# Performance work log

Measured on AMD Instinct MI355X. Metric: run time of the kernel, lower is better.

## Reference

```python
import jax, jax.numpy as jnp
import numpy as np

B, S, D, H = 4, 2048, 1024, 16
HD = D // H

def setup_inputs() -> dict:
    key = jax.random.key(0)
    ks = jax.random.split(key, 5)
    x = jax.random.normal(ks[0], (B, S, D), dtype=jnp.float32)
    # learned params (torch Linear: y = x @ W.T + b)
    s1 = 1.0 / np.sqrt(D)
    Wqkv = jax.random.uniform(ks[1], (3 * D, D), jnp.float32, -s1, s1)
    bqkv = jax.random.uniform(ks[2], (3 * D,), jnp.float32, -s1, s1)
    Wproj = jax.random.uniform(ks[3], (D, D), jnp.float32, -s1, s1)
    bproj = jax.random.uniform(ks[4], (D,), jnp.float32, -s1, s1)
    # causal mask, broadcast over batch and heads; 0 -> masked
    mask = jnp.tril(jnp.ones((S, S), jnp.int32))[None, None]
    return {"x": x, "Wqkv": Wqkv, "bqkv": bqkv, "Wproj": Wproj, "bproj": bproj, "mask": mask}

def reference(x, Wqkv, bqkv, Wproj, bproj, mask):
    b, s, d = x.shape
    qkv = x @ Wqkv.T + bqkv                      # [B,S,3D]
    qkv = qkv.reshape(b, s, 3, H, HD).transpose(2, 0, 3, 1, 4)  # [3,B,H,S,HD]
    q, k, v = qkv[0], qkv[1], qkv[2]
    scores = jnp.einsum('bhqd,bhkd->bhqk', q, k) / np.sqrt(HD).astype(np.float32)
    scores = jnp.where(mask == 0, -jnp.inf, scores)
    attn = jax.nn.softmax(scores, axis=-1)
    ctx = jnp.einsum('bhqk,bhkd->bhqd', attn, v)  # [B,H,S,HD]
    ctx = ctx.transpose(0, 2, 1, 3).reshape(b, s, d)
    return ctx @ Wproj.T + bproj
```

## Files before the change

kernel.cpp:

```cpp
#include <hip/hip_runtime.h>
#include <stdint.h>

typedef __bf16 bf16;
typedef __bf16 bf16x4 __attribute__((ext_vector_type(4)));
typedef __bf16 bf16x8 __attribute__((ext_vector_type(8)));
typedef float f32x4 __attribute__((ext_vector_type(4)));
typedef short short4v __attribute__((ext_vector_type(4)));

#define NB 4
#define NS 2048
#define ND 1024
#define NH 16
#define NHD 64
#define QSCALE 0.1803368801111204f
#define FMAX   8.0f

typedef const __attribute__((address_space(1))) unsigned GU;
typedef __attribute__((address_space(3))) unsigned LU;

#define WAIT_VM(n) asm volatile("s_waitcnt vmcnt(" #n ")" ::: "memory")
#define BAR() do { asm volatile("" ::: "memory"); __builtin_amdgcn_s_barrier(); \
                   asm volatile("" ::: "memory"); } while (0)

__device__ __forceinline__ bf16x8 load8f(const float* p) {
    float4 a = *(const float4*)p;
    float4 b = *(const float4*)(p + 4);
    bf16x8 r;
    r[0] = (bf16)a.x; r[1] = (bf16)a.y; r[2] = (bf16)a.z; r[3] = (bf16)a.w;
    r[4] = (bf16)b.x; r[5] = (bf16)b.y; r[6] = (bf16)b.z; r[7] = (bf16)b.w;
    return r;
}
__device__ __forceinline__ void store8(bf16* p, bf16x8 v) { *(bf16x8*)p = v; }
__device__ __forceinline__ void store8(float* p, bf16x8 v) {
    float4 a; a.x = (float)v[0]; a.y = (float)v[1]; a.z = (float)v[2]; a.w = (float)v[3];
    float4 b; b.x = (float)v[4]; b.y = (float)v[5]; b.z = (float)v[6]; b.w = (float)v[7];
    *(float4*)p = a; *(float4*)(p + 4) = b;
}

__device__ __forceinline__ f32x4 mfma16(bf16x4 a, bf16x4 b, f32x4 c) {
#ifdef __HIP_DEVICE_COMPILE__
#if __has_builtin(__builtin_amdgcn_mfma_f32_16x16x16bf16_1k)
    return __builtin_amdgcn_mfma_f32_16x16x16bf16_1k(
        __builtin_bit_cast(short4v, a), __builtin_bit_cast(short4v, b), c, 0, 0, 0);
#else
    f32x4 d;
    asm("v_mfma_f32_16x16x16_bf16 %0, %1, %2, %3"
        : "=v"(d) : "v"(a), "v"(b), "v"(c));
    return d;
#endif
#else
    return c;
#endif
}

__device__ __forceinline__ int sw(int row, int col) {
    return row * 72 + (col ^ (((row >> 2) & 3) * 16));
}

__global__ __launch_bounds__(256)
void convert_kernel(const float* __restrict__ s0, bf16* __restrict__ d0, int n0,
                    const float* __restrict__ s1, bf16* __restrict__ d1, int n1,
                    const float* __restrict__ s2, bf16* __restrict__ d2, int n2)
{
    int idx = (blockIdx.x * 256 + threadIdx.x) * 8;
    const float* s; bf16* d;
    if (idx < n0)              { s = s0 + idx;  d = d0 + idx; }
    else if ((idx -= n0) < n1) { s = s1 + idx;  d = d1 + idx; }
    else if ((idx -= n1) < n2) { s = s2 + idx;  d = d2 + idx; }
    else return;
    *(bf16x8*)d = load8f(s);
}

template<typename TO, int MODE>
__device__ __forceinline__ void epi256(
    f32x4 (&acc)[4][4], bf16* Ls, const float* __restrict__ bias,
    TO* __restrict__ O0, bf16* __restrict__ O1, bf16* __restrict__ O2,
    int N, int m0, int n0, int tid)
{
    const int lane = tid & 63;
    const int w = tid >> 6, wm = w >> 2, wn = w & 3;
    const int lr = lane & 15, quad = lane >> 4;
    const int cls = (MODE == 0) ? (n0 >> 10) : 1;

    if (MODE == 0 && cls == 2) {
#pragma unroll
        for (int im = 0; im < 4; ++im) {
            int rowb = wm * 64 + im * 16 + quad * 4;
#pragma unroll
            for (int in = 0; in < 4; ++in) {
                int col = wn * 64 + in * 16 + lr;
                float bv = bias[n0 + col];
                bf16x4 pv;
#pragma unroll
                for (int r = 0; r < 4; ++r) pv[r] = (bf16)(acc[im][in][r] + bv);
                *(bf16x4*)&Ls[col * 136 + rowb] = pv;
            }
        }
        __syncthreads();
        const int b = m0 >> 11, s0 = m0 & 2047;
#pragma unroll
        for (int p = 0; p < 8; ++p) {
            int idx = tid + 512 * p;
            int col = idx >> 4, mg = idx & 15;
            bf16x8 v8 = *(const bf16x8*)&Ls[col * 136 + mg * 8];
            int ncol = n0 + col;
            int h = (ncol >> 6) & 15, hd = ncol & 63;
            *(bf16x8*)&((bf16*)O0)[((size_t)(b * NH + h) * NHD + hd) * NS + s0 + mg * 8] = v8;
        }
    } else {
#pragma unroll
        for (int im = 0; im < 4; ++im) {
            int rowb = wm * 64 + im * 16 + quad * 4;
#pragma unroll
            for (int in = 0; in < 4; ++in) {
                int col = wn * 64 + in * 16 + lr;
                float bv = bias[n0 + col];
#pragma unroll
                for (int r = 0; r < 4; ++r) {
                    float v = acc[im][in][r] + bv;
                    if (MODE == 0 && cls == 0) v *= QSCALE;
                    Ls[(rowb + r) * 264 + col] = (bf16)v;
                }
            }
        }
        __syncthreads();
#pragma unroll
        for (int p = 0; p < 8; ++p) {
            int idx = tid + 512 * p;
            int row = idx >> 5, colg = (idx & 31) * 8;
            bf16x8 v8 = *(const bf16x8*)&Ls[row * 264 + colg];
            if (MODE == 0) {
                int ncol = n0 + colg;
                int h = (ncol >> 6) & 15, hd = ncol & 63;
                int m = m0 + row, b = m >> 11, s = m & 2047;
                bf16* dst = (cls == 0) ? O1 : O2;
                *(bf16x8*)&dst[((size_t)(b * NH + h) * NS + s) * NHD + hd] = v8;
            } else {
                store8(&O0[(size_t)(m0 + row) * N + n0 + colg], v8);
            }
        }
    }
}

template<typename TO, int MODE>
__global__ __launch_bounds__(512, 2)
void gemm256(const bf16* __restrict__ Xp, const bf16* __restrict__ Wp,
             const float* __restrict__ bias, TO* __restrict__ O0,
             bf16* __restrict__ O1, bf16* __restrict__ O2, int N, int K)
{
    __shared__ __align__(16) bf16 L[49152];
    const int tid  = threadIdx.x;
    const int lane = tid & 63;
    const int w    = tid >> 6;
    const int lr   = lane & 15, quad = lane >> 4;
    const int wm   = w >> 2, wn = w & 3;
    const int m0   = blockIdx.y * 128;
    const int n0   = blockIdx.x * 256;

    const int lanep = lane ^ ((lane >> 3) & 7);
    const bf16* gsrc[6]; int ldst[6];
#pragma unroll
    for (int j = 0; j < 6; ++j) {
        int g = w * 6 + j;
        int isA = g < 16;
        int gb = isA ? g : g - 16;
        int c = gb * 64 + lanep;
        int grow = c >> 3, gcol = (c & 7) * 8;
        gsrc[j] = (isA ? Xp + (size_t)(m0 + grow) * K
                       : Wp + (size_t)(n0 + grow) * K) + gcol;
        ldst[j] = (isA ? 0 : 8192) + gb * 512;
    }

#define STAGE256(t) do { const int kofs_ = (t) * 64;                           \
    bf16* Lb_ = &L[((t) & 1) * 24576];                                         \
    _Pragma("unroll")                                                          \
    for (int j = 0; j < 6; ++j)                                                \
        __builtin_amdgcn_global_load_lds((GU*)(gsrc[j] + kofs_),               \
                                         (LU*)&Lb_[ldst[j]], 16, 0, 0); } while (0)

    const int cxor = (lr & 7) * 8;
    const int col0 = (0 * 32 + quad * 8) ^ cxor;
    const int col1 = (1 * 32 + quad * 8) ^ cxor;
    const int arow0 = (wm * 64 + lr) * 64;
    const int brow0 = 8192 + (wn * 64 + lr) * 64;

    f32x4 acc[4][4] = {};
    const int NT = K >> 6;

    STAGE256(0);
    STAGE256(1);
    WAIT_VM(6);
    BAR();

    for (int t = 0; t < NT; ++t) {
        const int db = (t & 1) * 24576;
        bf16x8 afr[2][4], bfr[2][4];
#pragma unroll
        for (int i = 0; i < 4; ++i) {
            afr[0][i] = *(const bf16x8*)&L[db + arow0 + i * 1024 + col0];
            afr[1][i] = *(const bf16x8*)&L[db + arow0 + i * 1024 + col1];
            bfr[0][i] = *(const bf16x8*)&L[db + brow0 + i * 1024 + col0];
            bfr[1][i] = *(const bf16x8*)&L[db + brow0 + i * 1024 + col1];
        }
        __builtin_amdgcn_s_setprio(1);
#pragma unroll
        for (int ks = 0; ks < 2; ++ks)
#pragma unroll
            for (int im = 0; im < 4; ++im)
#pragma unroll
                for (int in = 0; in < 4; ++in)
                    acc[im][in] = __builtin_amdgcn_mfma_f32_16x16x32_bf16(
                        afr[ks][im], bfr[ks][in], acc[im][in], 0, 0, 0);
        __builtin_amdgcn_s_setprio(0);
        BAR();
        if (t + 2 < NT) { STAGE256(t + 2); WAIT_VM(6); }
        else WAIT_VM(0);
        BAR();
    }

    epi256<TO, MODE>(acc, L, bias, O0, O1, O2, N, m0, n0, tid);
}
#undef STAGE256

__global__ __launch_bounds__(256, 3)
void attn_kernel(const bf16* __restrict__ Q, const bf16* __restrict__ K,
                 const bf16* __restrict__ Vt_g, bf16* __restrict__ ctx)
{
    const int jt = 15 - (blockIdx.x >> 6);
    const int bh = blockIdx.x & 63;
    const int b  = bh >> 4, h = bh & 15;
    const int q0 = jt * 128;
    const bf16* Qp = Q + (size_t)bh * NS * NHD;
    const bf16* Kp = K + (size_t)bh * NS * NHD;
    const bf16* Vp = Vt_g + (size_t)bh * NHD * NS;

    __shared__ union {
        struct { bf16 Kh[64 * 72]; bf16 Vh[64 * 72]; } s;
        bf16 QO[128 * 72];
    } u;

    const int tid  = threadIdx.x;
    const int lane = tid & 63;
    const int w    = tid >> 6;
    const int lr   = lane & 15, quad = lane >> 4;

    const int srow = tid >> 3;
    const int sch  = (tid & 7) * 8;

    bf16x8 kreg[2], vreg[2];
#pragma unroll
    for (int i = 0; i < 2; ++i) {
        kreg[i] = *(const bf16x8*)(Kp + (size_t)(srow + 32 * i) * NHD + sch);
        vreg[i] = *(const bf16x8*)(Vp + (size_t)(srow + 32 * i) * NS + sch);
    }

#pragma unroll
    for (int i = 0; i < 4; ++i) {
        int row = srow + 32 * i;
        *(bf16x8*)(&u.QO[sw(row, sch)]) =
            *(const bf16x8*)(Qp + (size_t)(q0 + row) * NHD + sch);
    }
    __syncthreads();

    bf16x8 qf[2][2];
#pragma unroll
    for (int qg = 0; qg < 2; ++qg)
#pragma unroll
        for (int ks = 0; ks < 2; ++ks)
            qf[qg][ks] = *(const bf16x8*)(&u.QO[sw(w * 32 + qg * 16 + lr, ks * 32 + quad * 8)]);
    __syncthreads();

    float l_part[2] = {0.f, 0.f};
    f32x4 acco[2][4] = {};

    const int wq0 = q0 + w * 32;
    const int nkt = 2 * jt + 2;
    for (int kt = 0; kt < nkt; ++kt) {
#pragma unroll
        for (int i = 0; i < 2; ++i) {
            *(bf16x8*)(&u.s.Kh[sw(srow + 32 * i, sch)]) = kreg[i];
            *(bf16x8*)(&u.s.Vh[sw(srow + 32 * i, sch)]) = vreg[i];
        }
        if (kt + 1 < nkt) {
#pragma unroll
            for (int i = 0; i < 2; ++i) {
                kreg[i] = *(const bf16x8*)(Kp + (size_t)((kt + 1) * 64 + srow + 32 * i) * NHD + sch);
                vreg[i] = *(const bf16x8*)(Vp + (size_t)(srow + 32 * i) * NS + (kt + 1) * 64 + sch);
            }
        }
        __syncthreads();

        if (kt * 64 <= wq0 + 31) {
            f32x4 sacc[2][4] = {};
#pragma unroll
            for (int ks = 0; ks < 2; ++ks) {
#pragma unroll
                for (int kn = 0; kn < 4; ++kn) {
                    bf16x8 ak = *(const bf16x8*)(&u.s.Kh[sw(kn * 16 + lr, ks * 32 + quad * 8)]);
                    sacc[0][kn] = __builtin_amdgcn_mfma_f32_16x16x32_bf16(ak, qf[0][ks], sacc[0][kn], 0, 0, 0);
                    sacc[1][kn] = __builtin_amdgcn_mfma_f32_16x16x32_bf16(ak, qf[1][ks], sacc[1][kn], 0, 0, 0);
                }
            }

            const bool diag = (kt * 64 + 63 > wq0);
            bf16x4 pf[2][4];
#pragma unroll
            for (int qg = 0; qg < 2; ++qg) {
                const int qrow = wq0 + qg * 16 + lr;
#pragma unroll
                for (int kn = 0; kn < 4; ++kn) {
#pragma unroll
                    for (int r = 0; r < 4; ++r) {
                        float x = sacc[qg][kn][r];
                        if (diag) {
                            int kcol = kt * 64 + kn * 16 + quad * 4 + r;
                            x = (kcol <= qrow) ? x : -INFINITY;
                        }
                        float p = __builtin_amdgcn_exp2f(x - FMAX);
                        l_part[qg] += p;
                        pf[qg][kn][r] = (bf16)p;
                    }
                }
            }

#pragma unroll
            for (int kn = 0; kn < 4; ++kn) {
#pragma unroll
                for (int jn = 0; jn < 4; ++jn) {
                    bf16x4 av = *(const bf16x4*)(&u.s.Vh[sw(jn * 16 + lr, kn * 16 + quad * 4)]);
                    acco[0][jn] = mfma16(av, pf[0][kn], acco[0][jn]);
                    acco[1][jn] = mfma16(av, pf[1][kn], acco[1][jn]);
                }
            }
        }
        __syncthreads();
    }

    float rinv[2];
#pragma unroll
    for (int qg = 0; qg < 2; ++qg) {
        float l = l_part[qg];
        l += __shfl_xor(l, 16);
        l += __shfl_xor(l, 32);
        rinv[qg] = 1.0f / l;
    }

    __syncthreads();
#pragma unroll
    for (int qg = 0; qg < 2; ++qg)
#pragma unroll
        for (int jn = 0; jn < 4; ++jn) {
            bf16x4 pv;
#pragma unroll
            for (int r = 0; r < 4; ++r) pv[r] = (bf16)(acco[qg][jn][r] * rinv[qg]);
            *(bf16x4*)&u.QO[(w * 32 + qg * 16 + lr) * 72 + jn * 16 + quad * 4] = pv;
        }
    __syncthreads();
#pragma unroll
    for (int p = 0; p < 4; ++p) {
        int idx = tid + 256 * p;
        int row = idx >> 3, colg = (idx & 7) * 8;
        bf16x8 v8 = *(const bf16x8*)&u.QO[row * 72 + colg];
        *(bf16x8*)&ctx[((size_t)(b * NS) + q0 + row) * ND + h * NHD + colg] = v8;
    }
}

extern "C" void kernel_launch(void* const* d_in, const int* in_sizes, int n_in,
                              void* d_out, int out_size, void* d_ws, size_t ws_size,
                              hipStream_t stream) {
    const float* x     = (const float*)d_in[0];
    const float* Wqkv  = (const float*)d_in[1];
    const float* bqkv  = (const float*)d_in[2];
    const float* Wproj = (const float*)d_in[3];
    const float* bproj = (const float*)d_in[4];
    float* out = (float*)d_out;

    const size_t per = (size_t)NB * NH * NS * NHD;
    bf16* q_ws = (bf16*)d_ws;
    bf16* k_ws = q_ws + per;
    bf16* v_ws = k_ws + per;
    bf16* x_bf = v_ws + per;
    bf16* c_ws = x_bf;
    bf16* wq_bf = x_bf + per;
    bf16* wp_bf = wq_bf + (size_t)3 * ND * ND;

    const int n0 = NB * NS * ND;
    const int n1 = 3 * ND * ND;
    const int n2 = ND * ND;
    convert_kernel<<<(n0 + n1 + n2) / (256 * 8), 256, 0, stream>>>(
        x, x_bf, n0, Wqkv, wq_bf, n1, Wproj, wp_bf, n2);

    dim3 gq(3 * ND / 256, NB * NS / 128);
    gemm256<bf16, 0><<<gq, 512, 0, stream>>>(
        x_bf, wq_bf, bqkv, v_ws, q_ws, k_ws, 3 * ND, ND);

    attn_kernel<<<dim3(NB * NH * 16), 256, 0, stream>>>(q_ws, k_ws, v_ws, c_ws);

    dim3 gp(ND / 256, NB * NS / 128);
    gemm256<float, 1><<<gp, 512, 0, stream>>>(
        c_ws, wp_bf, bproj, out, nullptr, nullptr, ND, ND);
}
```

Before: 264.0 us.

## Add dedicated 256x256-tile QKV GEMM with interleaved LDS reads and MFMA phases

Replaces the generic 128x256 QKV GEMM with a dedicated kernel that computes 256x256 output tiles. It stages tiles with global_load_lds double buffering, splits each K-step into four barrier-separated fragment-load and MFMA phases, and raises wave priority around the MFMAs. The larger tile should cut global traffic per FLOP and improve operand reuse. The cost is 128 KB of LDS and many accumulator registers, and it halves the number of blocks, which may lower occupancy or leave compute units idle in the tail.

```diff
diff --git a/kernel.cpp b/kernel.cpp
--- a/kernel.cpp
+++ b/kernel.cpp
@@ -19,6 +19,8 @@
 typedef __attribute__((address_space(3))) unsigned LU;
 
 #define WAIT_VM(n) asm volatile("s_waitcnt vmcnt(" #n ")" ::: "memory")
+#define LGKM0() do { asm volatile("s_waitcnt lgkmcnt(0)" ::: "memory"); \
+                     __builtin_amdgcn_sched_barrier(0); } while (0)
 #define BAR() do { asm volatile("" ::: "memory"); __builtin_amdgcn_s_barrier(); \
                    asm volatile("" ::: "memory"); } while (0)
 
@@ -71,6 +73,175 @@
     *(bf16x8*)d = load8f(s);
 }
 
+__global__ __launch_bounds__(512, 2)
+void gemm_qkv(const bf16* __restrict__ Xp, const bf16* __restrict__ Wp,
+              const float* __restrict__ bias, bf16* __restrict__ OV,
+              bf16* __restrict__ OQ, bf16* __restrict__ OK, int K)
+{
+    __shared__ __align__(16) bf16 L[65536];
+    const int tid  = threadIdx.x;
+    const int lane = tid & 63;
+    const int w    = tid >> 6;
+    const int lr   = lane & 15, quad = lane >> 4;
+    const int wm   = w >> 2, wn = w & 3;
+    const int m0   = blockIdx.y * 256;
+    const int n0   = blockIdx.x * 256;
+
+    const int rb   = w * 32 + (lane >> 3);
+    const int scol = ((lane & 7) ^ (lane >> 3)) * 8;
+    const bf16* gA = Xp + (size_t)(m0 + rb) * K + scol;
+    const bf16* gB = Wp + (size_t)(n0 + rb) * K + scol;
+    const int sdA  = w * 2048;
+    const int sdB  = 16384 + w * 2048;
+
+#define STG(t) do { const int ko_ = (t) * 64;                                   \
+    bf16* Lb_ = &L[((t) & 1) * 32768];                                          \
+    _Pragma("unroll")                                                           \
+    for (int ip = 0; ip < 4; ++ip) {                                            \
+        __builtin_amdgcn_global_load_lds((GU*)(gA + (size_t)ip * 8 * K + ko_),  \
+                                         (LU*)&Lb_[sdA + ip * 512], 16, 0, 0);  \
+        __builtin_amdgcn_global_load_lds((GU*)(gB + (size_t)ip * 8 * K + ko_),  \
+                                         (LU*)&Lb_[sdB + ip * 512], 16, 0, 0);  \
+    } } while (0)
+
+    const int ck0  = ((quad) ^ (lr & 7)) * 8;
+    const int ck1  = ((4 + quad) ^ (lr & 7)) * 8;
+    const int arow = (wm * 128 + lr) * 64;
+    const int brow = 16384 + (wn * 64 + lr) * 64;
+
+    f32x4 acc[8][4] = {};
+    const int NT = K >> 6;
+
+    STG(0); STG(1);
+    WAIT_VM(8);
+    BAR();
+
+    for (int t = 0; t < NT; ++t) {
+        const int db = (t & 1) * 32768;
+        bf16x8 afr[4], bfr[4];
+#pragma unroll
+        for (int in = 0; in < 4; ++in) bfr[in] = *(const bf16x8*)&L[db + brow + in * 1024 + ck0];
+#pragma unroll
+        for (int im = 0; im < 4; ++im) afr[im] = *(const bf16x8*)&L[db + arow + im * 1024 + ck0];
+        BAR();
+        __builtin_amdgcn_s_setprio(1);
+#pragma unroll
+        for (int im = 0; im < 4; ++im)
+#pragma unroll
+            for (int in = 0; in < 4; ++in)
+                acc[im][in] = __builtin_amdgcn_mfma_f32_16x16x32_bf16(afr[im], bfr[in], acc[im][in], 0, 0, 0);
+        __builtin_amdgcn_s_setprio(0);
+        BAR();
+#pragma unroll
+        for (int im = 0; im < 4; ++im) afr[im] = *(const bf16x8*)&L[db + arow + (im + 4) * 1024 + ck0];
+        BAR();
+        __builtin_amdgcn_s_setprio(1);
+#pragma unroll
+        for (int im = 0; im < 4; ++im)
+#pragma unroll
+            for (int in = 0; in < 4; ++in)
+                acc[im + 4][in] = __builtin_amdgcn_mfma_f32_16x16x32_bf16(afr[im], bfr[in], acc[im + 4][in], 0, 0, 0);
+        __builtin_amdgcn_s_setprio(0);
+        BAR();
+#pragma unroll
+        for (int in = 0; in < 4; ++in) bfr[in] = *(const bf16x8*)&L[db + brow + in * 1024 + ck1];
+#pragma unroll
+        for (int im = 0; im < 4; ++im) afr[im] = *(const bf16x8*)&L[db + arow + im * 1024 + ck1];
+        BAR();
+        __builtin_amdgcn_s_setprio(1);
+#pragma unroll
+        for (int im = 0; im < 4; ++im)
+#pragma unroll
+            for (int in = 0; in < 4; ++in)
+                acc[im][in] = __builtin_amdgcn_mfma_f32_16x16x32_bf16(afr[im], bfr[in], acc[im][in], 0, 0, 0);
+        __builtin_amdgcn_s_setprio(0);
+        BAR();
+#pragma unroll
+        for (int im = 0; im < 4; ++im) afr[im] = *(const bf16x8*)&L[db + arow + (im + 4) * 1024 + ck1];
+        LGKM0();
+        BAR();
+        __builtin_amdgcn_s_setprio(1);
+#pragma unroll
+        for (int im = 0; im < 4; ++im)
+#pragma unroll
+            for (int in = 0; in < 4; ++in)
+                acc[im + 4][in] = __builtin_amdgcn_mfma_f32_16x16x32_bf16(afr[im], bfr[in], acc[im + 4][in], 0, 0, 0);
+        __builtin_amdgcn_s_setprio(0);
+        if (t + 2 < NT) { STG(t + 2); WAIT_VM(8); }
+        else WAIT_VM(0);
+        BAR();
+    }
+#undef STG
+
+    const int cls = n0 >> 10;
+    if (cls == 2) {
+        const int b = m0 >> 11, s0 = m0 & 2047;
+#pragma unroll
+        for (int ph = 0; ph < 2; ++ph) {
+            if (wm == ph) {
+#pragma unroll
+                for (int im = 0; im < 8; ++im) {
+                    int rowb = im * 16 + quad * 4;
+#pragma unroll
+                    for (int in = 0; in < 4; ++in) {
+                        int col = wn * 64 + in * 16 + lr;
+                        float bv = bias[n0 + col];
+                        bf16x4 pv;
+#pragma unroll
+                        for (int r = 0; r < 4; ++r) pv[r] = (bf16)(acc[im][in][r] + bv);
+                        *(bf16x4*)&L[col * 136 + rowb] = pv;
+                    }
+                }
+            }
+            __syncthreads();
+#pragma unroll
+            for (int p = 0; p < 8; ++p) {
+                int idx = tid + 512 * p;
+                int col = idx >> 4, mg = idx & 15;
+                bf16x8 v8 = *(const bf16x8*)&L[col * 136 + mg * 8];
+                int ncol = n0 + col;
+                int h = (ncol >> 6) & 15, hd = ncol & 63;
+                *(bf16x8*)&OV[((size_t)(b * NH + h) * NHD + hd) * NS + s0 + ph * 128 + mg * 8] = v8;
+            }
+            __syncthreads();
+        }
+    } else {
+#pragma unroll
+        for (int ph = 0; ph < 2; ++ph) {
+            if (wm == ph) {
+#pragma unroll
+                for (int im = 0; im < 8; ++im) {
+                    int rowb = im * 16 + quad * 4;
+#pragma unroll
+                    for (int in = 0; in < 4; ++in) {
+                        int col = wn * 64 + in * 16 + lr;
+                        float bv = bias[n0 + col];
+#pragma unroll
+                        for (int r = 0; r < 4; ++r) {
+                            float v = acc[im][in][r] + bv;
+                            if (cls == 0) v *= QSCALE;
+                            L[(rowb + r) * 264 + col] = (bf16)v;
+                        }
+                    }
+                }
+            }
+            __syncthreads();
+#pragma unroll
+            for (int p = 0; p < 8; ++p) {
+                int idx = tid + 512 * p;
+                int row = idx >> 5, colg = (idx & 31) * 8;
+                bf16x8 v8 = *(const bf16x8*)&L[row * 264 + colg];
+                int ncol = n0 + colg;
+                int h = (ncol >> 6) & 15, hd = ncol & 63;
+                int m = m0 + ph * 128 + row, b = m >> 11, s = m & 2047;
+                bf16* dst = (cls == 0) ? OQ : OK;
+                *(bf16x8*)&dst[((size_t)(b * NH + h) * NS + s) * NHD + hd] = v8;
+            }
+            __syncthreads();
+        }
+    }
+}
+
 template<typename TO, int MODE>
 __device__ __forceinline__ void epi256(
     f32x4 (&acc)[4][4], bf16* Ls, const float* __restrict__ bias,
@@ -390,9 +561,8 @@
     convert_kernel<<<(n0 + n1 + n2) / (256 * 8), 256, 0, stream>>>(
         x, x_bf, n0, Wqkv, wq_bf, n1, Wproj, wp_bf, n2);
 
-    dim3 gq(3 * ND / 256, NB * NS / 128);
-    gemm256<bf16, 0><<<gq, 512, 0, stream>>>(
-        x_bf, wq_bf, bqkv, v_ws, q_ws, k_ws, 3 * ND, ND);
+    dim3 gq(3 * ND / 256, NB * NS / 256);
+    gemm_qkv<<<gq, 512, 0, stream>>>(x_bf, wq_bf, bqkv, v_ws, q_ws, k_ws, ND);
 
     attn_kernel<<<dim3(NB * NH * 16), 256, 0, stream>>>(q_ws, k_ws, v_ws, c_ws);
 
```

Result: no change. 265.5 us (+0.6%).
